# Performance work log

Hardware: AMD Instinct MI355X
Metric: run time of the kernel (lower is better)

Reference implementation:

```python
import jax, jax.numpy as jnp
import numpy as np
from jax import lax

B, D, E, H, W = 256, 64, 16, 64, 64
PROJ, FC, NA = 512, 1024, 2

def _conv(x, w, pad):
    # x: [N,C,H,W], w: [O,I,kh,kw]
    return lax.conv_general_dilated(x, w, (1, 1), [(pad, pad), (pad, pad)],
                                    dimension_numbers=('NCHW', 'OIHW', 'NCHW'))

def _maxpool2(x):
    return lax.reduce_window(x, -jnp.inf, lax.max, (1, 1, 2, 2), (1, 1, 2, 2), 'VALID')

def _sample_conv(x, w, b):
    # per-sample conv with its own gathered expert weights: x [D,h,w], w [D,D,3,3]
    y = lax.conv_general_dilated(x[None], w, (1, 1), [(1, 1), (1, 1)],
                                 dimension_numbers=('NCHW', 'OIHW', 'NCHW'))[0]
    return y + b[:, None, None]

_expert_conv = jax.vmap(_sample_conv)  # batch of samples, each with its own kernel

def setup_inputs() -> dict:
    key = jax.random.key(0)
    ks = jax.random.split(key, 12)
    s = 0.05
    return {
        'image': jax.random.normal(ks[0], (B, 3, H, W), jnp.float32),
        'question': jax.random.randint(ks[1], (B, 8), 0, E),
        'stem_w0': jax.random.normal(ks[2], (D, 3, 3, 3), jnp.float32) * s,
        'stem_b0': jnp.zeros((D,), jnp.float32),
        'stem_w': jax.random.normal(ks[3], (3, D, D, 3, 3), jnp.float32) * s,
        'stem_b': jnp.zeros((3, D), jnp.float32),
        'exp_w1': jax.random.normal(ks[4], (E, D, D, 3, 3), jnp.float32) * s,
        'exp_b1': jnp.zeros((E, D), jnp.float32),
        'exp_w2': jax.random.normal(ks[5], (E, D, D, 3, 3), jnp.float32) * s,
        'exp_b2': jnp.zeros((E, D), jnp.float32),
        'proj_w': jax.random.normal(ks[6], (PROJ, D, 1, 1), jnp.float32) * s,
        'proj_b': jnp.zeros((PROJ,), jnp.float32),
        'fc1_w': jax.random.normal(ks[7], (FC, PROJ * 8 * 8), jnp.float32) * 0.01,
        'fc1_b': jnp.zeros((FC,), jnp.float32),
        'fc2_w': jax.random.normal(ks[8], (NA, FC), jnp.float32) * 0.01,
        'fc2_b': jnp.zeros((NA,), jnp.float32),
    }

def reference(image, question, stem_w0, stem_b0, stem_w, stem_b,
              exp_w1, exp_b1, exp_w2, exp_b2,
              proj_w, proj_b, fc1_w, fc1_b, fc2_w, fc2_b):
    # --- stem: 4 conv3x3 + ReLU, maxpool after layers 0 and 2 (64->32->16) ---
    h = jax.nn.relu(_conv(image, stem_w0, 1) + stem_b0[None, :, None, None])
    h = _maxpool2(h)
    h = jax.nn.relu(_conv(h, stem_w[0], 1) + stem_b[0][None, :, None, None])
    h = jax.nn.relu(_conv(h, stem_w[1], 1) + stem_b[1][None, :, None, None])
    h = _maxpool2(h)
    h = jax.nn.relu(_conv(h, stem_w[2], 1) + stem_b[2][None, :, None, None])
    # --- chain1 routing: cols (lhs=4, rel=5, rhs=7) each pick a ResidualBlock expert ---
    for col in (4, 5, 7):
        idx = question[:, col]                       # [B] expert ids
        w1, b1 = exp_w1[idx], exp_b1[idx]            # gather per-sample kernels
        w2, b2 = exp_w2[idx], exp_b2[idx]
        mid = jax.nn.relu(_expert_conv(h, w1, b1))   # conv1 + ReLU
        out = _expert_conv(mid, w2, b2)              # conv2 (no BN)
        h = jax.nn.relu(h + out)                     # residual + ReLU
    # --- classifier: 1x1 proj + ReLU, maxpool2, flatten, fc, fc ---
    c = jax.nn.relu(_conv(h, proj_w, 0) + proj_b[None, :, None, None])  # [B,512,16,16]
    c = _maxpool2(c)                                                     # [B,512,8,8]
    c = c.reshape(c.shape[0], -1)                                        # [B,32768]
    c = jax.nn.relu(c @ fc1_w.T + fc1_b)
    return c @ fc2_w.T + fc2_b                                           # [B,2]
```

## Files before the change

### kernel.cpp

```cpp
#include <hip/hip_runtime.h>
#include <cstddef>


typedef _Float16 half8 __attribute__((ext_vector_type(8)));
typedef _Float16 half4_t __attribute__((ext_vector_type(4)));
typedef float f32x4 __attribute__((ext_vector_type(4)));

#define LO_SCALE 2048.0f
#define LO_INV (1.0f / 2048.0f)

__global__ void transw_k(const float* __restrict__ src, float* __restrict__ dst,
                         int O, int I, int K, int total) {
    int id = blockIdx.x * 256 + threadIdx.x;
    if (id >= total) return;
    int OIK = O * I * K;
    int n = id / OIK, rem = id % OIK;
    int o = rem / (I * K), r2 = rem % (I * K);
    int i = r2 / K, k = r2 % K;
    dst[(size_t)n * OIK + (i * K + k) * O + o] = src[id];
}

__global__ void wxform_k(const float* __restrict__ src, _Float16* __restrict__ dst,
                         int nlayers) {
    int id = blockIdx.x * 256 + threadIdx.x;
    if (id >= nlayers * 36864) return;
    int layer = id / 36864, idx = id % 36864;
    int j = idx & 7, l = (idx >> 3) & 63, nt = (idx >> 9) & 3;
    int icc = (idx >> 11) & 1, tap = idx >> 12;
    int kl = (l >> 4) * 8 + j, ic = icc * 32 + kl, oc = nt * 16 + (l & 15);
    float v = src[(size_t)layer * 36864 + (oc * 64 + ic) * 9 + tap];
    _Float16 hi = (_Float16)v;
    _Float16 lo = (_Float16)((v - (float)hi) * LO_SCALE);
    dst[(size_t)layer * 73728 + idx] = hi;
    dst[(size_t)layer * 73728 + 36864 + idx] = lo;
}

__global__ void pwxform_k(const float* __restrict__ src, _Float16* __restrict__ dst) {
    int id = blockIdx.x * 256 + threadIdx.x;
    if (id >= 32768) return;
    int j = id & 7, l = (id >> 3) & 63, icc = (id >> 9) & 1, nt = id >> 10;
    int kl = (l >> 4) * 8 + j, ic = icc * 32 + kl, oc = nt * 16 + (l & 15);
    float v = src[oc * 64 + ic];
    _Float16 hi = (_Float16)v;
    _Float16 lo = (_Float16)((v - (float)hi) * LO_SCALE);
    dst[id] = hi;
    dst[32768 + id] = lo;
}

__global__ __launch_bounds__(256, 4)
void conv1_k(const float* __restrict__ img, const float* __restrict__ w0t,
             const float* __restrict__ b0, float* __restrict__ out) {
    int b = blockIdx.x, tile = blockIdx.y, ocg = blockIdx.z;
    int typ = (tile >> 1) * 16, txp = (tile & 1) * 16;
    int cy0 = typ * 2, cx0 = txp * 2;
    __shared__ float lds[3][34][34];
    const float* imb = img + (size_t)b * 3 * 64 * 64;
    for (int i = threadIdx.x; i < 3 * 34 * 34; i += 256) {
        int c = i / 1156, rem = i % 1156, r = rem / 34, cc = rem % 34;
        int gy = cy0 - 1 + r, gx = cx0 - 1 + cc;
        float v = 0.f;
        if (gy >= 0 && gy < 64 && gx >= 0 && gx < 64) v = imb[(c * 64 + gy) * 64 + gx];
        lds[c][r][cc] = v;
    }
    __syncthreads();
    int pyl = threadIdx.x >> 4, pxl = threadIdx.x & 15;
    float win[3][4][4];
#pragma unroll
    for (int c = 0; c < 3; ++c)
#pragma unroll
        for (int wy = 0; wy < 4; ++wy)
#pragma unroll
            for (int wx = 0; wx < 4; ++wx)
                win[c][wy][wx] = lds[c][2 * pyl + wy][2 * pxl + wx];
    int py = typ + pyl, px = txp + pxl;
    float* op = &out[(((size_t)b * 32 + py) * 32 + px) * 64];
#pragma unroll
    for (int q = 0; q < 4; ++q) {
        int ocq = ocg * 4 + q;
        float acc[4][4] = {};
#pragma unroll
        for (int c = 0; c < 3; ++c)
#pragma unroll
            for (int ky = 0; ky < 3; ++ky)
#pragma unroll
                for (int kx = 0; kx < 3; ++kx) {
                    float4 w = *(const float4*)&w0t[(c * 9 + ky * 3 + kx) * 64 + ocq * 4];
                    float wv4[4] = {w.x, w.y, w.z, w.w};
#pragma unroll
                    for (int p2 = 0; p2 < 4; ++p2) {
                        float iv = win[c][(p2 >> 1) + ky][(p2 & 1) + kx];
#pragma unroll
                        for (int o = 0; o < 4; ++o)
                            acc[p2][o] = fmaf(iv, wv4[o], acc[p2][o]);
                    }
                }
        float4 res;
        float* rp = (float*)&res;
#pragma unroll
        for (int o = 0; o < 4; ++o) {
            float bvv = b0[ocq * 4 + o];
            float m = fmaxf(fmaxf(acc[0][o], acc[1][o]), fmaxf(acc[2][o], acc[3][o]));
            rp[o] = fmaxf(m + bvv, 0.f);
        }
        *(float4*)&op[ocq * 4] = res;
    }
}

template <int S, bool POOL, bool RES>
__global__ __launch_bounds__(256, 2)
void convm_k(const float* __restrict__ in, float* __restrict__ out,
             const _Float16* __restrict__ wf, const float* __restrict__ bias,
             const float* __restrict__ res, const int* __restrict__ question,
             int qcol) {
    int b = blockIdx.x, t = blockIdx.y;
    constexpr int NTX = S / 16;
    int ty0 = (t / NTX) * 8, tx0 = (t % NTX) * 16;

    __shared__ __align__(16) _Float16 lds[2 * 7200];

    int tid = threadIdx.x, lane = tid & 63, wv = tid >> 6;
    const _Float16* wb = wf;
    const float* bb = bias;
    if (question) {
        int idx = question[b * 8 + qcol];
        wb += (size_t)idx * 73728;
        bb += idx * 64;
    }
    float bv[4];
#pragma unroll
    for (int nt = 0; nt < 4; ++nt) bv[nt] = bb[nt * 16 + (lane & 15)];

    f32x4 acc1[2][4] = {};
    f32x4 acc2[2][4] = {};

    int am = lane & 15;
    int k0 = (lane >> 4) * 8;

    for (int icc = 0; icc < 2; ++icc) {
        __syncthreads();
        for (int i = tid; i < 1440; i += 256) {
            int pix = i >> 3, j4 = i & 7;
            int hy = pix / 18, hx = pix % 18;
            int gy = ty0 + hy - 1, gx = tx0 + hx - 1;
            float4 v = {0.f, 0.f, 0.f, 0.f};
            if (gy >= 0 && gy < S && gx >= 0 && gx < S)
                v = *(const float4*)&in[(((size_t)b * S + gy) * S + gx) * 64 + icc * 32 + j4 * 4];
            _Float16 h0 = (_Float16)v.x, h1 = (_Float16)v.y;
            _Float16 h2 = (_Float16)v.z, h3 = (_Float16)v.w;
            half4_t hh = {h0, h1, h2, h3};
            half4_t ll = {(_Float16)((v.x - (float)h0) * LO_SCALE),
                          (_Float16)((v.y - (float)h1) * LO_SCALE),
                          (_Float16)((v.z - (float)h2) * LO_SCALE),
                          (_Float16)((v.w - (float)h3) * LO_SCALE)};
            *(half4_t*)&lds[pix * 40 + j4 * 4] = hh;
            *(half4_t*)&lds[7200 + pix * 40 + j4 * 4] = ll;
        }
        __syncthreads();

#pragma unroll
        for (int ky = 0; ky < 3; ++ky)
#pragma unroll
            for (int kx = 0; kx < 3; ++kx) {
                int tap = ky * 3 + kx;
                const _Float16* wp = wb + (tap * 2 + icc) * 2048 + lane * 8;
                half8 bhi[4], blo[4];
#pragma unroll
                for (int nt = 0; nt < 4; ++nt) {
                    bhi[nt] = *(const half8*)(wp + nt * 512);
                    blo[nt] = *(const half8*)(wp + nt * 512 + 36864);
                }
#pragma unroll
                for (int mt = 0; mt < 2; ++mt) {
                    int MT = wv * 2 + mt;
                    int Q = MT * 4 + (am >> 2), s = am & 3;
                    int py = (Q >> 3) * 2 + (s >> 1), px = (Q & 7) * 2 + (s & 1);
                    const _Float16* ap = &lds[((py + ky) * 18 + (px + kx)) * 40 + k0];
                    half8 ahi = *(const half8*)ap;
                    half8 alo = *(const half8*)(ap + 7200);
#pragma unroll
                    for (int nt = 0; nt < 4; ++nt) {
                        acc1[mt][nt] = __builtin_amdgcn_mfma_f32_16x16x32_f16(
                            ahi, bhi[nt], acc1[mt][nt], 0, 0, 0);
                        acc2[mt][nt] = __builtin_amdgcn_mfma_f32_16x16x32_f16(
                            ahi, blo[nt], acc2[mt][nt], 0, 0, 0);
                        acc2[mt][nt] = __builtin_amdgcn_mfma_f32_16x16x32_f16(
                            alo, bhi[nt], acc2[mt][nt], 0, 0, 0);
                    }
                }
            }
    }

    int cn = lane & 15, rq = lane >> 4;
#pragma unroll
    for (int mt = 0; mt < 2; ++mt) {
        int MT = wv * 2 + mt;
        int Q = MT * 4 + rq;
        int qy = Q >> 3, qx = Q & 7;
#pragma unroll
        for (int nt = 0; nt < 4; ++nt) {
            int oc = nt * 16 + cn;
            float vals[4];
#pragma unroll
            for (int r = 0; r < 4; ++r)
                vals[r] = acc1[mt][nt][r] + acc2[mt][nt][r] * LO_INV + bv[nt];
            if (POOL) {
                float m = fmaxf(fmaxf(vals[0], vals[1]), fmaxf(vals[2], vals[3]));
                m = fmaxf(m, 0.f);
                int opy = (ty0 >> 1) + qy, opx = (tx0 >> 1) + qx;
                out[(((size_t)b * (S / 2) + opy) * (S / 2) + opx) * 64 + oc] = m;
            } else {
#pragma unroll
                for (int r = 0; r < 4; ++r) {
                    int py = qy * 2 + (r >> 1), px = qx * 2 + (r & 1);
                    size_t o = (((size_t)b * S + (ty0 + py)) * S + (tx0 + px)) * 64 + oc;
                    float v = vals[r];
                    if (RES) v += res[o];
                    out[o] = fmaxf(v, 0.f);
                }
            }
        }
    }
}

__global__ __launch_bounds__(256)
void projm_k(const float* __restrict__ in ,
             const _Float16* __restrict__ pw, const float* __restrict__ bias,
             _Float16* __restrict__ outh ) {
    int b = blockIdx.x;
    __shared__ float lt[64 * 65];
    int tid = threadIdx.x, lane = tid & 63, wv = tid >> 6;
    int row = lane & 15, cseg = lane >> 4;

    half8 ah[4][2], al[4][2];
#pragma unroll
    for (int mt = 0; mt < 4; ++mt) {
        int MT = wv * 4 + mt;
        int Q = MT * 4 + (row >> 2), s = row & 3;
        int y = (Q >> 3) * 2 + (s >> 1), x = (Q & 7) * 2 + (s & 1);
        const float* ip = in + ((size_t)b * 256 + y * 16 + x) * 64 + cseg * 8;
#pragma unroll
        for (int icc = 0; icc < 2; ++icc) {
            float4 v0 = *(const float4*)(ip + icc * 32);
            float4 v1 = *(const float4*)(ip + icc * 32 + 4);
            _Float16 h0 = (_Float16)v0.x, h1 = (_Float16)v0.y;
            _Float16 h2 = (_Float16)v0.z, h3 = (_Float16)v0.w;
            _Float16 h4 = (_Float16)v1.x, h5 = (_Float16)v1.y;
            _Float16 h6 = (_Float16)v1.z, h7 = (_Float16)v1.w;
            ah[mt][icc] = (half8){h0, h1, h2, h3, h4, h5, h6, h7};
            al[mt][icc] = (half8){(_Float16)((v0.x - (float)h0) * LO_SCALE),
                                  (_Float16)((v0.y - (float)h1) * LO_SCALE),
                                  (_Float16)((v0.z - (float)h2) * LO_SCALE),
                                  (_Float16)((v0.w - (float)h3) * LO_SCALE),
                                  (_Float16)((v1.x - (float)h4) * LO_SCALE),
                                  (_Float16)((v1.y - (float)h5) * LO_SCALE),
                                  (_Float16)((v1.z - (float)h6) * LO_SCALE),
                                  (_Float16)((v1.w - (float)h7) * LO_SCALE)};
        }
    }

    for (int ogl = 0; ogl < 4; ++ogl) {
        int og = blockIdx.y * 4 + ogl;
        half8 bh[4][2], bl[4][2];
#pragma unroll
        for (int ntl = 0; ntl < 4; ++ntl)
#pragma unroll
            for (int icc = 0; icc < 2; ++icc) {
                int nt = og * 4 + ntl;
                const _Float16* wp = pw + ((nt * 2 + icc) * 64 + lane) * 8;
                bh[ntl][icc] = *(const half8*)wp;
                bl[ntl][icc] = *(const half8*)(wp + 32768);
            }
        f32x4 a1[4][4] = {};
        f32x4 a2[4][4] = {};
#pragma unroll
        for (int icc = 0; icc < 2; ++icc)
#pragma unroll
            for (int mt = 0; mt < 4; ++mt)
#pragma unroll
                for (int ntl = 0; ntl < 4; ++ntl) {
                    a1[mt][ntl] = __builtin_amdgcn_mfma_f32_16x16x32_f16(
                        ah[mt][icc], bh[ntl][icc], a1[mt][ntl], 0, 0, 0);
                    a2[mt][ntl] = __builtin_amdgcn_mfma_f32_16x16x32_f16(
                        ah[mt][icc], bl[ntl][icc], a2[mt][ntl], 0, 0, 0);
                    a2[mt][ntl] = __builtin_amdgcn_mfma_f32_16x16x32_f16(
                        al[mt][icc], bh[ntl][icc], a2[mt][ntl], 0, 0, 0);
                }
        if (ogl) __syncthreads();
#pragma unroll
        for (int mt = 0; mt < 4; ++mt) {
            int Qg = (wv * 4 + mt) * 4 + (lane >> 4);
#pragma unroll
            for (int ntl = 0; ntl < 4; ++ntl) {
                float bvv = bias[og * 64 + ntl * 16 + (lane & 15)];
                float v0 = a1[mt][ntl][0] + a2[mt][ntl][0] * LO_INV + bvv;
                float v1 = a1[mt][ntl][1] + a2[mt][ntl][1] * LO_INV + bvv;
                float v2 = a1[mt][ntl][2] + a2[mt][ntl][2] * LO_INV + bvv;
                float v3 = a1[mt][ntl][3] + a2[mt][ntl][3] * LO_INV + bvv;
                float m = fmaxf(fmaxf(fmaxf(v0, v1), fmaxf(v2, v3)), 0.f);
                lt[(ntl * 16 + (lane & 15)) * 65 + Qg] = m;
            }
        }
        __syncthreads();
#pragma unroll
        for (int r = 0; r < 16; ++r) {
            int f = r * 256 + tid;
            int ol = f >> 6, q = f & 63;
            float v = lt[ol * 65 + q];
            _Float16 h = (_Float16)v;
            _Float16 l = (_Float16)((v - (float)h) * LO_SCALE);
            size_t o = (size_t)b * 32768 + og * 4096 + ol * 64 + q;
            outh[o] = h;
            outh[8388608 + o] = l;
        }
    }
}

__global__ __launch_bounds__(256)
void fc1m_k(const _Float16* __restrict__ Ahl ,
            const float* __restrict__ W,
            float* __restrict__ partial ) {
    int bid = blockIdx.x;
    int lid = (bid & 7) * 64 + (bid >> 3);
    int mt = lid & 1, nt = (lid >> 1) & 7, ks = lid >> 4;
    int m0 = mt * 128, n0 = nt * 128;
    const _Float16* Ab = Ahl + (size_t)m0 * 32768 + ks * 1024;
    const float* Wb = W + (size_t)n0 * 32768 + ks * 1024;

    __shared__ __align__(16) _Float16 lds[40960];

    int tid = threadIdx.x, lane = tid & 63, wv = tid >> 6;
    int wm = (wv & 1) * 64, wn = (wv >> 1) * 64;
    int koff = (lane >> 4) * 8, fr = lane & 15;

    f32x4 acc1[4][4] = {};
    f32x4 acc2[4][4] = {};

    int arow[2], ak8[2];
#pragma unroll
    for (int p = 0; p < 2; ++p) {
        int idx = p * 256 + tid;
        arow[p] = idx >> 2;
        ak8[p] = (idx & 3) * 8;
    }
    int wrow[4], wc4[4];
#pragma unroll
    for (int p = 0; p < 4; ++p) {
        int idx = p * 256 + tid;
        wrow[p] = idx >> 3;
        wc4[p] = (idx & 7) << 2;
    }

    half8 pa_h[2], pa_l[2];
    float4 rw[4];

#pragma unroll
    for (int p = 0; p < 2; ++p) {
        pa_h[p] = *(const half8*)&Ab[(size_t)arow[p] * 32768 + ak8[p]];
        pa_l[p] = *(const half8*)&Ab[8388608 + (size_t)arow[p] * 32768 + ak8[p]];
    }
#pragma unroll
    for (int p = 0; p < 4; ++p)
        rw[p] = *(const float4*)&Wb[(size_t)wrow[p] * 32768 + wc4[p]];
    {
        _Float16* b0p = lds;
#pragma unroll
        for (int p = 0; p < 2; ++p) {
            *(half8*)&b0p[arow[p] * 40 + ak8[p]] = pa_h[p];
            *(half8*)&b0p[5120 + arow[p] * 40 + ak8[p]] = pa_l[p];
        }
#pragma unroll
        for (int p = 0; p < 4; ++p) {
            float4 u = rw[p];
            _Float16 g0 = (_Float16)u.x, g1 = (_Float16)u.y;
            _Float16 g2 = (_Float16)u.z, g3 = (_Float16)u.w;
            half4_t gh = {g0, g1, g2, g3};
            half4_t gl = {(_Float16)((u.x - (float)g0) * LO_SCALE),
                          (_Float16)((u.y - (float)g1) * LO_SCALE),
                          (_Float16)((u.z - (float)g2) * LO_SCALE),
                          (_Float16)((u.w - (float)g3) * LO_SCALE)};
            *(half4_t*)&b0p[10240 + wrow[p] * 40 + wc4[p]] = gh;
            *(half4_t*)&b0p[15360 + wrow[p] * 40 + wc4[p]] = gl;
        }
    }
#pragma unroll
    for (int p = 0; p < 2; ++p) {
        pa_h[p] = *(const half8*)&Ab[(size_t)arow[p] * 32768 + 32 + ak8[p]];
        pa_l[p] = *(const half8*)&Ab[8388608 + (size_t)arow[p] * 32768 + 32 + ak8[p]];
    }
#pragma unroll
    for (int p = 0; p < 4; ++p)
        rw[p] = *(const float4*)&Wb[(size_t)wrow[p] * 32768 + 32 + wc4[p]];
    __syncthreads();

    for (int kt = 0; kt < 32; ++kt) {
        _Float16* cur = lds + (kt & 1) * 20480;
        _Float16* nxt = lds + ((kt + 1) & 1) * 20480;
        if (kt < 31) {
#pragma unroll
            for (int p = 0; p < 2; ++p) {
                *(half8*)&nxt[arow[p] * 40 + ak8[p]] = pa_h[p];
                *(half8*)&nxt[5120 + arow[p] * 40 + ak8[p]] = pa_l[p];
            }
#pragma unroll
            for (int p = 0; p < 4; ++p) {
                float4 u = rw[p];
                _Float16 g0 = (_Float16)u.x, g1 = (_Float16)u.y;
                _Float16 g2 = (_Float16)u.z, g3 = (_Float16)u.w;
                half4_t gh = {g0, g1, g2, g3};
                half4_t gl = {(_Float16)((u.x - (float)g0) * LO_SCALE),
                              (_Float16)((u.y - (float)g1) * LO_SCALE),
                              (_Float16)((u.z - (float)g2) * LO_SCALE),
                              (_Float16)((u.w - (float)g3) * LO_SCALE)};
                *(half4_t*)&nxt[10240 + wrow[p] * 40 + wc4[p]] = gh;
                *(half4_t*)&nxt[15360 + wrow[p] * 40 + wc4[p]] = gl;
            }
            if (kt < 30) {
                int kb = (kt + 2) * 32;
#pragma unroll
                for (int p = 0; p < 2; ++p) {
                    pa_h[p] = *(const half8*)&Ab[(size_t)arow[p] * 32768 + kb + ak8[p]];
                    pa_l[p] = *(const half8*)&Ab[8388608 + (size_t)arow[p] * 32768 + kb + ak8[p]];
                }
#pragma unroll
                for (int p = 0; p < 4; ++p)
                    rw[p] = *(const float4*)&Wb[(size_t)wrow[p] * 32768 + kb + wc4[p]];
            }
        }
        half8 bh[4], bl[4];
#pragma unroll
        for (int nf = 0; nf < 4; ++nf) {
            int r = wn + nf * 16 + fr;
            bh[nf] = *(const half8*)&cur[10240 + r * 40 + koff];
            bl[nf] = *(const half8*)&cur[15360 + r * 40 + koff];
        }
#pragma unroll
        for (int mf = 0; mf < 4; ++mf) {
            int r = wm + mf * 16 + fr;
            half8 ah = *(const half8*)&cur[r * 40 + koff];
            half8 al = *(const half8*)&cur[5120 + r * 40 + koff];
#pragma unroll
            for (int nf = 0; nf < 4; ++nf) {
                acc1[mf][nf] = __builtin_amdgcn_mfma_f32_16x16x32_f16(
                    ah, bh[nf], acc1[mf][nf], 0, 0, 0);
                acc2[mf][nf] = __builtin_amdgcn_mfma_f32_16x16x32_f16(
                    ah, bl[nf], acc2[mf][nf], 0, 0, 0);
                acc2[mf][nf] = __builtin_amdgcn_mfma_f32_16x16x32_f16(
                    al, bh[nf], acc2[mf][nf], 0, 0, 0);
            }
        }
        __syncthreads();
    }

    int rq = lane >> 4, cn = lane & 15;
    float* pb = partial + (size_t)ks * 262144;
#pragma unroll
    for (int mf = 0; mf < 4; ++mf)
#pragma unroll
        for (int nf = 0; nf < 4; ++nf) {
            int n = n0 + wn + nf * 16 + cn;
#pragma unroll
            for (int r = 0; r < 4; ++r) {
                int m = m0 + wm + mf * 16 + rq * 4 + r;
                pb[(size_t)m * 1024 + n] = acc1[mf][nf][r] + acc2[mf][nf][r] * LO_INV;
            }
        }
}

__global__ __launch_bounds__(256)
void fc1red_k(const float* __restrict__ partial, const float* __restrict__ b1,
              float* __restrict__ fc1o_t ) {
    int m = blockIdx.x;
    int n0 = threadIdx.x * 4;
    float4 s = {0.f, 0.f, 0.f, 0.f};
    for (int ks = 0; ks < 32; ++ks) {
        float4 v = *(const float4*)&partial[((size_t)ks * 256 + m) * 1024 + n0];
        s.x += v.x; s.y += v.y; s.z += v.z; s.w += v.w;
    }
    fc1o_t[(size_t)(n0 + 0) * 256 + m] = fmaxf(s.x + b1[n0 + 0], 0.f);
    fc1o_t[(size_t)(n0 + 1) * 256 + m] = fmaxf(s.y + b1[n0 + 1], 0.f);
    fc1o_t[(size_t)(n0 + 2) * 256 + m] = fmaxf(s.z + b1[n0 + 2], 0.f);
    fc1o_t[(size_t)(n0 + 3) * 256 + m] = fmaxf(s.w + b1[n0 + 3], 0.f);
}

__global__ __launch_bounds__(256)
void fc2a_k(const float* __restrict__ a_t, const float* __restrict__ W2,
            float* __restrict__ p2) {
    int n2 = blockIdx.x, ks = blockIdx.y;
    int m = threadIdx.x;
    float acc = 0.f;
    for (int k = ks * 256; k < ks * 256 + 256; ++k)
        acc = fmaf(a_t[(size_t)k * 256 + m], W2[n2 * 1024 + k], acc);
    p2[((size_t)n2 * 4 + ks) * 256 + m] = acc;
}

__global__ __launch_bounds__(512)
void fc2b_k(const float* __restrict__ p2, const float* __restrict__ b2,
            float* __restrict__ out) {
    int i = threadIdx.x;
    int m = i >> 1, n2 = i & 1;
    float s = b2[n2];
#pragma unroll
    for (int ks = 0; ks < 4; ++ks) s += p2[((size_t)n2 * 4 + ks) * 256 + m];
    out[m * 2 + n2] = s;
}

extern "C" void kernel_launch(void* const* d_in, const int* in_sizes, int n_in,
                              void* d_out, int out_size, void* d_ws, size_t ws_size,
                              hipStream_t stream) {
    const float* image   = (const float*)d_in[0];
    const int*   question= (const int*)d_in[1];
    const float* stem_w0 = (const float*)d_in[2];
    const float* stem_b0 = (const float*)d_in[3];
    const float* stem_w  = (const float*)d_in[4];
    const float* stem_b  = (const float*)d_in[5];
    const float* exp_w1  = (const float*)d_in[6];
    const float* exp_b1  = (const float*)d_in[7];
    const float* exp_w2  = (const float*)d_in[8];
    const float* exp_b2  = (const float*)d_in[9];
    const float* proj_w  = (const float*)d_in[10];
    const float* proj_b  = (const float*)d_in[11];
    const float* fc1_w   = (const float*)d_in[12];
    const float* fc1_b   = (const float*)d_in[13];
    const float* fc2_w   = (const float*)d_in[14];
    const float* fc2_b   = (const float*)d_in[15];
    (void)in_sizes; (void)n_in; (void)out_size; (void)ws_size;

    float* ws = (float*)d_ws;
    const size_t A = 16777216, P2N = 4194304;
    float* p1    = ws;
    float* h2    = ws + A;
    float* p2    = ws + 2 * A;
    float* wtr   = ws + 2 * A + P2N;
    float* w0t   = wtr;
    _Float16* pwF = (_Float16*)(wtr + 1728);
    float* pfc2  = wtr + 1728 + 32768;
    _Float16* f16b = (_Float16*)(wtr + 36544);
    _Float16* stemtF = f16b;
    _Float16* e1tF   = f16b + 3 * 73728;
    _Float16* e2tF   = e1tF + 16 * 73728;
    float* hA    = ws;
    float* hB    = ws + P2N;
    float* hC    = ws + 2 * P2N;
    _Float16* pool3h = (_Float16*)h2;
    float* fc1o  = h2 + 8388608;
    float* fc1p  = ws;

    transw_k<<<(1728 + 255) / 256, 256, 0, stream>>>(stem_w0, w0t, 64, 3, 9, 1728);
    pwxform_k<<<128, 256, 0, stream>>>(proj_w, pwF);
    wxform_k<<<(3 * 36864 + 255) / 256, 256, 0, stream>>>(stem_w, stemtF, 3);
    wxform_k<<<(16 * 36864 + 255) / 256, 256, 0, stream>>>(exp_w1, e1tF, 16);
    wxform_k<<<(16 * 36864 + 255) / 256, 256, 0, stream>>>(exp_w2, e2tF, 16);

    conv1_k<<<dim3(256, 4, 4), 256, 0, stream>>>(image, w0t, stem_b0, p1);
    convm_k<32, false, false><<<dim3(256, 8), 256, 0, stream>>>(
        p1, h2, stemtF, stem_b, nullptr, nullptr, 0);
    convm_k<32, true, false><<<dim3(256, 8), 256, 0, stream>>>(
        h2, p2, stemtF + 73728, stem_b + 64, nullptr, nullptr, 0);
    convm_k<16, false, false><<<dim3(256, 2), 256, 0, stream>>>(
        p2, hA, stemtF + 2 * 73728, stem_b + 128, nullptr, nullptr, 0);

    const int cols[3] = {4, 5, 7};
    float* hin = hA;
    float* hmid = hB;
    float* hout = hC;
    for (int r = 0; r < 3; ++r) {
        convm_k<16, false, false><<<dim3(256, 2), 256, 0, stream>>>(
            hin, hmid, e1tF, exp_b1, nullptr, question, cols[r]);
        convm_k<16, false, true><<<dim3(256, 2), 256, 0, stream>>>(
            hmid, hout, e2tF, exp_b2, hin, question, cols[r]);
        float* tp = hin; hin = hout; hout = hmid; hmid = tp;
    }

    projm_k<<<dim3(256, 2), 256, 0, stream>>>(hin, pwF, proj_b, pool3h);
    fc1m_k<<<512, 256, 0, stream>>>(pool3h, fc1_w, fc1p);
    fc1red_k<<<256, 256, 0, stream>>>(fc1p, fc1_b, fc1o);
    fc2a_k<<<dim3(2, 4), 256, 0, stream>>>(fc1o, fc2_w, pfc2);
    fc2b_k<<<1, 512, 0, stream>>>(pfc2, fc2_b, (float*)d_out);
}
```

Measured before the change: 468.4 us.

## Store inter-layer activations as split fp16 hi/lo planes instead of fp32

```diff
diff --git a/kernel.cpp b/kernel.cpp
--- a/kernel.cpp
+++ b/kernel.cpp
@@ -49,7 +49,8 @@
 
 __global__ __launch_bounds__(256, 4)
 void conv1_k(const float* __restrict__ img, const float* __restrict__ w0t,
-             const float* __restrict__ b0, float* __restrict__ out) {
+             const float* __restrict__ b0, _Float16* __restrict__ out) {
+    const size_t NE1 = 16777216;
     int b = blockIdx.x, tile = blockIdx.y, ocg = blockIdx.z;
     int typ = (tile >> 1) * 16, txp = (tile & 1) * 16;
     int cy0 = typ * 2, cx0 = txp * 2;
@@ -73,7 +74,7 @@
             for (int wx = 0; wx < 4; ++wx)
                 win[c][wy][wx] = lds[c][2 * pyl + wy][2 * pxl + wx];
     int py = typ + pyl, px = txp + pxl;
-    float* op = &out[(((size_t)b * 32 + py) * 32 + px) * 64];
+    size_t obase = (((size_t)b * 32 + py) * 32 + px) * 64;
 #pragma unroll
     for (int q = 0; q < 4; ++q) {
         int ocq = ocg * 4 + q;
@@ -94,24 +95,29 @@
                             acc[p2][o] = fmaf(iv, wv4[o], acc[p2][o]);
                     }
                 }
-        float4 res;
-        float* rp = (float*)&res;
+        half4_t rh, rl;
 #pragma unroll
         for (int o = 0; o < 4; ++o) {
             float bvv = b0[ocq * 4 + o];
             float m = fmaxf(fmaxf(acc[0][o], acc[1][o]), fmaxf(acc[2][o], acc[3][o]));
-            rp[o] = fmaxf(m + bvv, 0.f);
-        }
-        *(float4*)&op[ocq * 4] = res;
+            float v = fmaxf(m + bvv, 0.f);
+            _Float16 h = (_Float16)v;
+            rh[o] = h;
+            rl[o] = (_Float16)((v - (float)h) * LO_SCALE);
+        }
+        *(half4_t*)&out[obase + ocq * 4] = rh;
+        *(half4_t*)&out[NE1 + obase + ocq * 4] = rl;
     }
 }
 
 template <int S, bool POOL, bool RES>
 __global__ __launch_bounds__(256, 2)
-void convm_k(const float* __restrict__ in, float* __restrict__ out,
+void convm_k(const _Float16* __restrict__ in, _Float16* __restrict__ out,
              const _Float16* __restrict__ wf, const float* __restrict__ bias,
-             const float* __restrict__ res, const int* __restrict__ question,
+             const _Float16* __restrict__ res, const int* __restrict__ question,
              int qcol) {
+    constexpr size_t NEin = (size_t)S * S * 64 * 256;
+    constexpr size_t NEout = POOL ? NEin / 4 : NEin;
     int b = blockIdx.x, t = blockIdx.y;
     constexpr int NTX = S / 16;
     int ty0 = (t / NTX) * 8, tx0 = (t % NTX) * 16;
@@ -138,22 +144,18 @@
 
     for (int icc = 0; icc < 2; ++icc) {
         __syncthreads();
-        for (int i = tid; i < 1440; i += 256) {
-            int pix = i >> 3, j4 = i & 7;
+        for (int i = tid; i < 720; i += 256) {
+            int pix = i >> 2, j8 = (i & 3) * 8;
             int hy = pix / 18, hx = pix % 18;
             int gy = ty0 + hy - 1, gx = tx0 + hx - 1;
-            float4 v = {0.f, 0.f, 0.f, 0.f};
-            if (gy >= 0 && gy < S && gx >= 0 && gx < S)
-                v = *(const float4*)&in[(((size_t)b * S + gy) * S + gx) * 64 + icc * 32 + j4 * 4];
-            _Float16 h0 = (_Float16)v.x, h1 = (_Float16)v.y;
-            _Float16 h2 = (_Float16)v.z, h3 = (_Float16)v.w;
-            half4_t hh = {h0, h1, h2, h3};
-            half4_t ll = {(_Float16)((v.x - (float)h0) * LO_SCALE),
-                          (_Float16)((v.y - (float)h1) * LO_SCALE),
-                          (_Float16)((v.z - (float)h2) * LO_SCALE),
-                          (_Float16)((v.w - (float)h3) * LO_SCALE)};
-            *(half4_t*)&lds[pix * 40 + j4 * 4] = hh;
-            *(half4_t*)&lds[7200 + pix * 40 + j4 * 4] = ll;
+            half8 vh = {}, vl = {};
+            if (gy >= 0 && gy < S && gx >= 0 && gx < S) {
+                size_t src = (((size_t)b * S + gy) * S + gx) * 64 + icc * 32 + j8;
+                vh = *(const half8*)&in[src];
+                vl = *(const half8*)&in[NEin + src];
+            }
+            *(half8*)&lds[pix * 40 + j8] = vh;
+            *(half8*)&lds[7200 + pix * 40 + j8] = vl;
         }
         __syncthreads();
 
@@ -207,15 +209,21 @@
                 float m = fmaxf(fmaxf(vals[0], vals[1]), fmaxf(vals[2], vals[3]));
                 m = fmaxf(m, 0.f);
                 int opy = (ty0 >> 1) + qy, opx = (tx0 >> 1) + qx;
-                out[(((size_t)b * (S / 2) + opy) * (S / 2) + opx) * 64 + oc] = m;
+                size_t o = (((size_t)b * (S / 2) + opy) * (S / 2) + opx) * 64 + oc;
+                _Float16 h = (_Float16)m;
+                out[o] = h;
+                out[NEout + o] = (_Float16)((m - (float)h) * LO_SCALE);
             } else {
 #pragma unroll
                 for (int r = 0; r < 4; ++r) {
                     int py = qy * 2 + (r >> 1), px = qx * 2 + (r & 1);
                     size_t o = (((size_t)b * S + (ty0 + py)) * S + (tx0 + px)) * 64 + oc;
                     float v = vals[r];
-                    if (RES) v += res[o];
-                    out[o] = fmaxf(v, 0.f);
+                    if (RES) v += (float)res[o] + (float)res[NEin + o] * LO_INV;
+                    v = fmaxf(v, 0.f);
+                    _Float16 h = (_Float16)v;
+                    out[o] = h;
+                    out[NEout + o] = (_Float16)((v - (float)h) * LO_SCALE);
                 }
             }
         }
@@ -223,9 +231,10 @@
 }
 
 __global__ __launch_bounds__(256)
-void projm_k(const float* __restrict__ in ,
+void projm_k(const _Float16* __restrict__ in ,
              const _Float16* __restrict__ pw, const float* __restrict__ bias,
              _Float16* __restrict__ outh ) {
+    const size_t NE2 = 4194304;
     int b = blockIdx.x;
     __shared__ float lt[64 * 65];
     int tid = threadIdx.x, lane = tid & 63, wv = tid >> 6;
@@ -237,24 +246,11 @@
         int MT = wv * 4 + mt;
         int Q = MT * 4 + (row >> 2), s = row & 3;
         int y = (Q >> 3) * 2 + (s >> 1), x = (Q & 7) * 2 + (s & 1);
-        const float* ip = in + ((size_t)b * 256 + y * 16 + x) * 64 + cseg * 8;
+        size_t pb = ((size_t)b * 256 + y * 16 + x) * 64 + cseg * 8;
 #pragma unroll
         for (int icc = 0; icc < 2; ++icc) {
-            float4 v0 = *(const float4*)(ip + icc * 32);
-            float4 v1 = *(const float4*)(ip + icc * 32 + 4);
-            _Float16 h0 = (_Float16)v0.x, h1 = (_Float16)v0.y;
-            _Float16 h2 = (_Float16)v0.z, h3 = (_Float16)v0.w;
-            _Float16 h4 = (_Float16)v1.x, h5 = (_Float16)v1.y;
-            _Float16 h6 = (_Float16)v1.z, h7 = (_Float16)v1.w;
-            ah[mt][icc] = (half8){h0, h1, h2, h3, h4, h5, h6, h7};
-            al[mt][icc] = (half8){(_Float16)((v0.x - (float)h0) * LO_SCALE),
-                                  (_Float16)((v0.y - (float)h1) * LO_SCALE),
-                                  (_Float16)((v0.z - (float)h2) * LO_SCALE),
-                                  (_Float16)((v0.w - (float)h3) * LO_SCALE),
-                                  (_Float16)((v1.x - (float)h4) * LO_SCALE),
-                                  (_Float16)((v1.y - (float)h5) * LO_SCALE),
-                                  (_Float16)((v1.z - (float)h6) * LO_SCALE),
-                                  (_Float16)((v1.w - (float)h7) * LO_SCALE)};
+            ah[mt][icc] = *(const half8*)&in[pb + icc * 32];
+            al[mt][icc] = *(const half8*)&in[NE2 + pb + icc * 32];
         }
     }
 
@@ -527,9 +523,6 @@
 
     float* ws = (float*)d_ws;
     const size_t A = 16777216, P2N = 4194304;
-    float* p1    = ws;
-    float* h2    = ws + A;
-    float* p2    = ws + 2 * A;
     float* wtr   = ws + 2 * A + P2N;
     float* w0t   = wtr;
     _Float16* pwF = (_Float16*)(wtr + 1728);
@@ -538,11 +531,14 @@
     _Float16* stemtF = f16b;
     _Float16* e1tF   = f16b + 3 * 73728;
     _Float16* e2tF   = e1tF + 16 * 73728;
-    float* hA    = ws;
-    float* hB    = ws + P2N;
-    float* hC    = ws + 2 * P2N;
-    _Float16* pool3h = (_Float16*)h2;
-    float* fc1o  = h2 + 8388608;
+    _Float16* p1h  = (_Float16*)ws;
+    _Float16* h2h  = (_Float16*)(ws + A);
+    _Float16* p2h  = (_Float16*)(ws + 2 * A);
+    _Float16* hAh  = (_Float16*)ws;
+    _Float16* hBh  = (_Float16*)(ws + P2N);
+    _Float16* hCh  = (_Float16*)(ws + 2 * P2N);
+    _Float16* pool3h = (_Float16*)(ws + A);
+    float* fc1o  = ws + A + 8388608;
     float* fc1p  = ws;
 
     transw_k<<<(1728 + 255) / 256, 256, 0, stream>>>(stem_w0, w0t, 64, 3, 9, 1728);
@@ -551,24 +547,24 @@
     wxform_k<<<(16 * 36864 + 255) / 256, 256, 0, stream>>>(exp_w1, e1tF, 16);
     wxform_k<<<(16 * 36864 + 255) / 256, 256, 0, stream>>>(exp_w2, e2tF, 16);
 
-    conv1_k<<<dim3(256, 4, 4), 256, 0, stream>>>(image, w0t, stem_b0, p1);
+    conv1_k<<<dim3(256, 4, 4), 256, 0, stream>>>(image, w0t, stem_b0, p1h);
     convm_k<32, false, false><<<dim3(256, 8), 256, 0, stream>>>(
-        p1, h2, stemtF, stem_b, nullptr, nullptr, 0);
+        p1h, h2h, stemtF, stem_b, nullptr, nullptr, 0);
     convm_k<32, true, false><<<dim3(256, 8), 256, 0, stream>>>(
-        h2, p2, stemtF + 73728, stem_b + 64, nullptr, nullptr, 0);
+        h2h, p2h, stemtF + 73728, stem_b + 64, nullptr, nullptr, 0);
     convm_k<16, false, false><<<dim3(256, 2), 256, 0, stream>>>(
-        p2, hA, stemtF + 2 * 73728, stem_b + 128, nullptr, nullptr, 0);
+        p2h, hAh, stemtF + 2 * 73728, stem_b + 128, nullptr, nullptr, 0);
 
     const int cols[3] = {4, 5, 7};
-    float* hin = hA;
-    float* hmid = hB;
-    float* hout = hC;
+    _Float16* hin = hAh;
+    _Float16* hmid = hBh;
+    _Float16* hout = hCh;
     for (int r = 0; r < 3; ++r) {
         convm_k<16, false, false><<<dim3(256, 2), 256, 0, stream>>>(
             hin, hmid, e1tF, exp_b1, nullptr, question, cols[r]);
         convm_k<16, false, true><<<dim3(256, 2), 256, 0, stream>>>(
             hmid, hout, e2tF, exp_b2, hin, question, cols[r]);
-        float* tp = hin; hin = hout; hout = hmid; hmid = tp;
+        _Float16* tp = hin; hin = hout; hout = hmid; hmid = tp;
     }
 
     projm_k<<<dim3(256, 2), 256, 0, stream>>>(hin, pwF, proj_b, pool3h);
```

New measurement: 464.3 us. No clear change (-0.9%).
